# Kernel tuning notes

Hardware: AMD Instinct MI355X
Metric: run time of the kernel (lower is better)

Reference implementation:

```python
import jax, jax.numpy as jnp
import numpy as np

B = 32      # batch
N = 1024    # input_size (= maxval)
EPS = 1.0   # regularization_strength


def _isotonic_l2(y):
    """Non-increasing isotonic regression (L2) of each row of y: [B, n].

    Uses the minimax characterization  sol_i = min_{j<=i} max_{k>=i} mean(y[j..k]),
    which equals the PAV solution and yields the correct block-averaging Jacobian
    under autodiff. O(n^2) memory per row, fully vectorized.
    """
    b, n = y.shape
    cs = jnp.concatenate([jnp.zeros((b, 1), y.dtype), jnp.cumsum(y, axis=-1)], axis=-1)  # [B, n+1]
    j = jnp.arange(n)[:, None]   # start index
    k = jnp.arange(n)[None, :]   # end index
    length = (k - j + 1).astype(y.dtype)
    # M[b, j, k] = mean(y[b, j..k]) for k >= j
    M = (cs[:, None, 1:] - cs[:, :-1, None]) / jnp.where(k >= j, length, jnp.ones_like(length))
    M = jnp.where(k >= j, M, -jnp.inf)
    # Amax[b, j, i] = max_{k >= i} M[b, j, k]  (suffix max along k)
    Amax = jax.lax.cummax(M, axis=2, reverse=True)
    # restrict to j <= i, then minimize over j
    Amax = jnp.where(j <= k, Amax, jnp.inf)  # here the k-axis plays the role of i
    return jnp.min(Amax, axis=1)  # [B, n]


def _soft_rank(x, eps):
    """fast-soft-sort soft_rank, direction=ASCENDING, regularization='l2'."""
    b, n = x.shape
    theta = x / eps
    perm = jnp.argsort(-theta, axis=-1)                 # descending sort permutation
    s = jnp.take_along_axis(theta, perm, axis=-1)       # sorted (descending)
    w = jnp.arange(n, 0, -1, dtype=x.dtype)             # [n, n-1, ..., 1]
    sol = _isotonic_l2(s - w)                           # dual solution
    primal = s - sol                                    # projection, sorted order
    inv = jnp.argsort(perm, axis=-1)
    return jnp.take_along_axis(primal, inv, axis=-1)    # unpermute -> ranks in [1, n]


def setup_inputs() -> dict:
    key = jax.random.key(0)
    x = jax.random.normal(key, (B, N), dtype=jnp.float32)
    return {"x": x}


def reference(x) -> jnp.ndarray:
    ranks = _soft_rank(x, EPS)                          # [B, n]
    n = x.shape[1]
    t = jnp.arange(1, n + 1, dtype=x.dtype)             # rank targets 1..n
    # out[b, j, i] = relu(1 - |ranks[b, j] - (i + 1)|)  (== torch .permute(0, 2, 1) result)
    return jax.nn.relu(1.0 - jnp.abs(ranks[:, :, None] - t[None, None, :]))
```

## Files before the change

kernel.cpp:

```cpp
#include <hip/hip_runtime.h>
#include <stdint.h>

#define N 1024
#define BATCH 32
#define NFILL 4096

__global__ __launch_bounds__(256) void count_kernel(const float* __restrict__ x,
                                                    int* __restrict__ pos_g) {
    __shared__ uint64_t keys[N];
    __shared__ int      partial[256];

    const int row   = blockIdx.x >> 4;
    const int chunk = blockIdx.x & 15;
    const int t     = threadIdx.x;

    const float4 xq = reinterpret_cast<const float4*>(x + row * N)[t];
    {
        const float vv[4] = {xq.x, xq.y, xq.z, xq.w};
        const int j0 = t << 2;
        #pragma unroll
        for (int e = 0; e < 4; ++e) {
            uint32_t u = __float_as_uint(vv[e]);
            u ^= (u & 0x80000000u) ? 0xFFFFFFFFu : 0x80000000u;
            keys[j0 + e] = (((uint64_t)u) << 10) | (uint64_t)(1023 - (j0 + e));
        }
    }
    __syncthreads();

    const int e = (chunk << 6) + (t & 63);
    const int q = t >> 6;
    const uint64_t kk = keys[e];
    const int kbeg = q << 8;
    int c = 0;
    #pragma unroll 4
    for (int k = kbeg; k < kbeg + 256; k += 4) {
        c += (int)(keys[k    ] > kk);
        c += (int)(keys[k + 1] > kk);
        c += (int)(keys[k + 2] > kk);
        c += (int)(keys[k + 3] > kk);
    }
    partial[t] = c;
    __syncthreads();

    if (t < 64)
        pos_g[row * N + e] = partial[t] + partial[t + 64] + partial[t + 128] + partial[t + 192];
}

__global__ __launch_bounds__(256) void fused_ranks_fill(const float* __restrict__ x,
                                                        const int* __restrict__ pos_g,
                                                        float* __restrict__ ranks,
                                                        float* __restrict__ out) {
    if (blockIdx.x >= BATCH) {
        const int fid = blockIdx.x - BATCH;
        float4* o = reinterpret_cast<float4*>(out) + (size_t)fid * 2048 + threadIdx.x;
        const float4 z = make_float4(0.0f, 0.0f, 0.0f, 0.0f);
        #pragma unroll
        for (int i = 0; i < 8; ++i) o[i * 256] = z;
        return;
    }

    __shared__ float    ss[N];
    __shared__ float    yv[N];
    __shared__ double   csum[N];
    __shared__ int      segid[N];
    __shared__ int      run_start[N+1];
    __shared__ float    run_mean[N];
    __shared__ double   stk_sum[N];
    __shared__ int      stk_cnt[N];
    __shared__ int      stk_runs[N];
    __shared__ double   wsumD[4];
    __shared__ int      wsumI[4];

    const int b = blockIdx.x;
    const int t = threadIdx.x;
    const int j0 = t << 2;
    const int lane = t & 63;
    const int wid = t >> 6;

    const float4 xq = reinterpret_cast<const float4*>(x + b * N)[t];
    const int4   pq = reinterpret_cast<const int4*>(pos_g + b * N)[t];
    ss[pq.x] = xq.x; ss[pq.y] = xq.y; ss[pq.z] = xq.z; ss[pq.w] = xq.w;
    __syncthreads();

    float4 yq;
    {
        const float4 sq = reinterpret_cast<const float4*>(ss)[t];
        yq.x = sq.x + (float)(j0 - 512);
        yq.y = sq.y + (float)(j0 - 511);
        yq.z = sq.z + (float)(j0 - 510);
        yq.w = sq.w + (float)(j0 - 509);
        reinterpret_cast<float4*>(yv)[t] = yq;
    }
    __syncthreads();

    const float ye[4] = {yq.x, yq.y, yq.z, yq.w};
    int    fl[4];
    int    lf[4];
    double lys[4];
    {
        float prev = (j0 == 0) ? -1.0e30f : yv[j0 - 1];
        double accy = 0.0; int accf = 0;
        #pragma unroll
        for (int e = 0; e < 4; ++e) {
            const int f = (prev > ye[e]) ? 1 : 0;
            prev = ye[e];
            fl[e] = f;
            accf += f;             lf[e]  = accf;
            accy += (double)ye[e]; lys[e] = accy;
        }
    }
    double vy = lys[3]; int vf = lf[3];
    #pragma unroll
    for (int off = 1; off < 64; off <<= 1) {
        const double oy = __shfl_up(vy, off);
        const int    of = __shfl_up(vf, off);
        if (lane >= off) { vy += oy; vf += of; }
    }
    if (lane == 63) { wsumD[wid] = vy; wsumI[wid] = vf; }
    __syncthreads();
    {
        double basey = vy - lys[3]; int basef = vf - lf[3];
        for (int w = 0; w < wid; ++w) { basey += wsumD[w]; basef += wsumI[w]; }
        #pragma unroll
        for (int e = 0; e < 4; ++e) {
            const int p   = j0 + e;
            const int seg = basef + lf[e];
            segid[p] = seg;
            csum[p]  = basey + lys[e];
            if (fl[e]) run_start[seg] = p;
        }
        if (t == 0) run_start[0] = 0;
    }
    __syncthreads();

    if (t == 0) {
        const int R = segid[N - 1] + 1;
        run_start[R] = N;
        int sp = 0;
        for (int r = 0; r < R; ++r) {
            const int a   = run_start[r];
            const int bnd = run_start[r + 1];
            double s = csum[bnd - 1] - ((a > 0) ? csum[a - 1] : 0.0);
            int    c = bnd - a;
            int    nr = 1;
            while (sp > 0 && s * (double)stk_cnt[sp - 1] > stk_sum[sp - 1] * (double)c) {
                s  += stk_sum[sp - 1];
                c  += stk_cnt[sp - 1];
                nr += stk_runs[sp - 1];
                --sp;
            }
            stk_sum[sp] = s; stk_cnt[sp] = c; stk_runs[sp] = nr; ++sp;
        }
        int rc = 0;
        for (int e2 = 0; e2 < sp; ++e2) {
            const float m = (float)(stk_sum[e2] / (double)stk_cnt[e2]);
            for (int q2 = 0; q2 < stk_runs[e2]; ++q2) run_mean[rc++] = m;
        }
    }
    __syncthreads();

    float4 r4;
    r4.x = xq.x - run_mean[segid[pq.x]] + 512.0f;
    r4.y = xq.y - run_mean[segid[pq.y]] + 512.0f;
    r4.z = xq.z - run_mean[segid[pq.z]] + 512.0f;
    r4.w = xq.w - run_mean[segid[pq.w]] + 512.0f;
    reinterpret_cast<float4*>(ranks + b * N)[t] = r4;
}

__global__ __launch_bounds__(256) void scatter_kernel(const float* __restrict__ ranks,
                                                      float* __restrict__ out) {
    const int row = blockIdx.x * 256 + threadIdx.x;
    const float r = ranks[row];
    const float f = floorf(r);
    const int   i1 = (int)f;
    const float frac = r - f;
    float* o = out + (size_t)row * N;
    if (i1 >= 1 && i1 <= N) o[i1 - 1] = 1.0f - frac;
    if (i1 >= 0 && i1 <  N) o[i1]     = frac;
}

extern "C" void kernel_launch(void* const* d_in, const int* in_sizes, int n_in,
                              void* d_out, int out_size, void* d_ws, size_t ws_size,
                              hipStream_t stream) {
    const float* x = (const float*)d_in[0];
    float* out = (float*)d_out;
    int*   pos_g = (int*)d_ws;
    float* ranks = (float*)d_ws + BATCH * N;

    count_kernel<<<BATCH * 16, 256, 0, stream>>>(x, pos_g);
    fused_ranks_fill<<<BATCH + NFILL, 256, 0, stream>>>(x, pos_g, ranks, out);
    scatter_kernel<<<(BATCH * N) / 256, 256, 0, stream>>>(ranks, out);
}
```

Measured before the change: 140.0 us.

## Fuse count, ranks and scatter into one kernel with atomic fill barrier

Merges the rank-counting kernel and the scatter kernel into the fused ranks/fill kernel. Each of the 32 row blocks now does the full O(N^2) comparison count itself, and the fill blocks each zero four times more data. Row blocks spin on a global atomic counter until all zero-fill blocks finish, then write the two non-zero entries directly. This removes two kernel launches and the intermediate buffers, but it serialises the counting onto 32 blocks and relies on all fill blocks making progress while row blocks spin, which is a deadlock risk if residency is limited.

```diff
diff --git a/kernel.cpp b/kernel.cpp
--- a/kernel.cpp
+++ b/kernel.cpp
@@ -3,62 +3,29 @@
 
 #define N 1024
 #define BATCH 32
-#define NFILL 4096
+#define NFILL 1024
 
-__global__ __launch_bounds__(256) void count_kernel(const float* __restrict__ x,
-                                                    int* __restrict__ pos_g) {
-    __shared__ uint64_t keys[N];
-    __shared__ int      partial[256];
-
-    const int row   = blockIdx.x >> 4;
-    const int chunk = blockIdx.x & 15;
-    const int t     = threadIdx.x;
-
-    const float4 xq = reinterpret_cast<const float4*>(x + row * N)[t];
-    {
-        const float vv[4] = {xq.x, xq.y, xq.z, xq.w};
-        const int j0 = t << 2;
-        #pragma unroll
-        for (int e = 0; e < 4; ++e) {
-            uint32_t u = __float_as_uint(vv[e]);
-            u ^= (u & 0x80000000u) ? 0xFFFFFFFFu : 0x80000000u;
-            keys[j0 + e] = (((uint64_t)u) << 10) | (uint64_t)(1023 - (j0 + e));
-        }
-    }
-    __syncthreads();
-
-    const int e = (chunk << 6) + (t & 63);
-    const int q = t >> 6;
-    const uint64_t kk = keys[e];
-    const int kbeg = q << 8;
-    int c = 0;
-    #pragma unroll 4
-    for (int k = kbeg; k < kbeg + 256; k += 4) {
-        c += (int)(keys[k    ] > kk);
-        c += (int)(keys[k + 1] > kk);
-        c += (int)(keys[k + 2] > kk);
-        c += (int)(keys[k + 3] > kk);
-    }
-    partial[t] = c;
-    __syncthreads();
-
-    if (t < 64)
-        pos_g[row * N + e] = partial[t] + partial[t + 64] + partial[t + 128] + partial[t + 192];
+__global__ __launch_bounds__(64) void init_kernel(int* __restrict__ counter) {
+    if (threadIdx.x == 0) *counter = 0;
 }
 
-__global__ __launch_bounds__(256) void fused_ranks_fill(const float* __restrict__ x,
-                                                        const int* __restrict__ pos_g,
-                                                        float* __restrict__ ranks,
-                                                        float* __restrict__ out) {
+__global__ __launch_bounds__(256) void mega_kernel(const float* __restrict__ x,
+                                                   float* __restrict__ out,
+                                                   int* __restrict__ counter) {
     if (blockIdx.x >= BATCH) {
         const int fid = blockIdx.x - BATCH;
-        float4* o = reinterpret_cast<float4*>(out) + (size_t)fid * 2048 + threadIdx.x;
+        float4* o = reinterpret_cast<float4*>(out) + (size_t)fid * 8192 + threadIdx.x;
         const float4 z = make_float4(0.0f, 0.0f, 0.0f, 0.0f);
         #pragma unroll
-        for (int i = 0; i < 8; ++i) o[i * 256] = z;
+        for (int i = 0; i < 32; ++i) o[i * 256] = z;
+        __threadfence();
+        __syncthreads();
+        if (threadIdx.x == 0)
+            __hip_atomic_fetch_add(counter, 1, __ATOMIC_RELEASE, __HIP_MEMORY_SCOPE_AGENT);
         return;
     }
 
+    __shared__ uint64_t keys[N];
     __shared__ float    ss[N];
     __shared__ float    yv[N];
     __shared__ double   csum[N];
@@ -78,8 +45,34 @@
     const int wid = t >> 6;
 
     const float4 xq = reinterpret_cast<const float4*>(x + b * N)[t];
-    const int4   pq = reinterpret_cast<const int4*>(pos_g + b * N)[t];
-    ss[pq.x] = xq.x; ss[pq.y] = xq.y; ss[pq.z] = xq.z; ss[pq.w] = xq.w;
+    const float vv[4] = {xq.x, xq.y, xq.z, xq.w};
+    uint64_t kk[4];
+    {
+        #pragma unroll
+        for (int e = 0; e < 4; ++e) {
+            uint32_t u = __float_as_uint(vv[e]);
+            u ^= (u & 0x80000000u) ? 0xFFFFFFFFu : 0x80000000u;
+            kk[e] = (((uint64_t)u) << 10) | (uint64_t)(1023 - (j0 + e));
+            keys[j0 + e] = kk[e];
+        }
+    }
+    __syncthreads();
+
+    int c[4] = {0, 0, 0, 0};
+    for (int k = 0; k < N; k += 4) {
+        const uint64_t k0 = keys[k];
+        const uint64_t k1 = keys[k + 1];
+        const uint64_t k2 = keys[k + 2];
+        const uint64_t k3 = keys[k + 3];
+        #pragma unroll
+        for (int e = 0; e < 4; ++e) {
+            c[e] += (int)(k0 > kk[e]);
+            c[e] += (int)(k1 > kk[e]);
+            c[e] += (int)(k2 > kk[e]);
+            c[e] += (int)(k3 > kk[e]);
+        }
+    }
+    ss[c[0]] = xq.x; ss[c[1]] = xq.y; ss[c[2]] = xq.z; ss[c[3]] = xq.w;
     __syncthreads();
 
     float4 yq;
@@ -141,15 +134,15 @@
             const int a   = run_start[r];
             const int bnd = run_start[r + 1];
             double s = csum[bnd - 1] - ((a > 0) ? csum[a - 1] : 0.0);
-            int    c = bnd - a;
+            int    cc = bnd - a;
             int    nr = 1;
-            while (sp > 0 && s * (double)stk_cnt[sp - 1] > stk_sum[sp - 1] * (double)c) {
+            while (sp > 0 && s * (double)stk_cnt[sp - 1] > stk_sum[sp - 1] * (double)cc) {
                 s  += stk_sum[sp - 1];
-                c  += stk_cnt[sp - 1];
+                cc += stk_cnt[sp - 1];
                 nr += stk_runs[sp - 1];
                 --sp;
             }
-            stk_sum[sp] = s; stk_cnt[sp] = c; stk_runs[sp] = nr; ++sp;
+            stk_sum[sp] = s; stk_cnt[sp] = cc; stk_runs[sp] = nr; ++sp;
         }
         int rc = 0;
         for (int e2 = 0; e2 < sp; ++e2) {
@@ -159,24 +152,22 @@
     }
     __syncthreads();
 
-    float4 r4;
-    r4.x = xq.x - run_mean[segid[pq.x]] + 512.0f;
-    r4.y = xq.y - run_mean[segid[pq.y]] + 512.0f;
-    r4.z = xq.z - run_mean[segid[pq.z]] + 512.0f;
-    r4.w = xq.w - run_mean[segid[pq.w]] + 512.0f;
-    reinterpret_cast<float4*>(ranks + b * N)[t] = r4;
-}
+    if (t == 0) {
+        while (__hip_atomic_load(counter, __ATOMIC_ACQUIRE, __HIP_MEMORY_SCOPE_AGENT) < NFILL)
+            __builtin_amdgcn_s_sleep(8);
+    }
+    __syncthreads();
 
-__global__ __launch_bounds__(256) void scatter_kernel(const float* __restrict__ ranks,
-                                                      float* __restrict__ out) {
-    const int row = blockIdx.x * 256 + threadIdx.x;
-    const float r = ranks[row];
-    const float f = floorf(r);
-    const int   i1 = (int)f;
-    const float frac = r - f;
-    float* o = out + (size_t)row * N;
-    if (i1 >= 1 && i1 <= N) o[i1 - 1] = 1.0f - frac;
-    if (i1 >= 0 && i1 <  N) o[i1]     = frac;
+    #pragma unroll
+    for (int e = 0; e < 4; ++e) {
+        const float r = vv[e] - run_mean[segid[c[e]]] + 512.0f;
+        const float f = floorf(r);
+        const int   i1 = (int)f;
+        const float frac = r - f;
+        float* o = out + (size_t)(b * N + j0 + e) * N;
+        if (i1 >= 1 && i1 <= N) o[i1 - 1] = 1.0f - frac;
+        if (i1 >= 0 && i1 <  N) o[i1]     = frac;
+    }
 }
 
 extern "C" void kernel_launch(void* const* d_in, const int* in_sizes, int n_in,
@@ -184,10 +175,8 @@
                               hipStream_t stream) {
     const float* x = (const float*)d_in[0];
     float* out = (float*)d_out;
-    int*   pos_g = (int*)d_ws;
-    float* ranks = (float*)d_ws + BATCH * N;
+    int* counter = (int*)d_ws;
 
-    count_kernel<<<BATCH * 16, 256, 0, stream>>>(x, pos_g);
-    fused_ranks_fill<<<BATCH + NFILL, 256, 0, stream>>>(x, pos_g, ranks, out);
-    scatter_kernel<<<(BATCH * N) / 256, 256, 0, stream>>>(ranks, out);
+    init_kernel<<<1, 64, 0, stream>>>(counter);
+    mega_kernel<<<BATCH + NFILL, 256, 0, stream>>>(x, out, counter);
 }
```

Result: slower. 298.4 us (+113.2%).
